# Performance work log

Hardware: AMD Instinct MI355X
Metric: run time of the kernel (lower is better)

Reference implementation:

```python
import jax, jax.numpy as jnp
from jax import lax
import numpy as np

K = 5          # conv / pool / box-filter kernel size
PAD = 2        # padding used everywhere in the module (same-size for K=5)
CO, DO = 16, 16
ROUTING = 3


def _squash(p, axis):
    # squash(p) from the source, applied along capsule-dim axis
    nsq = jnp.sum(p * p, axis=axis, keepdims=True)
    return nsq / (1.0 + nsq) * p / jnp.sqrt(nsq + 1e-9)


def setup_inputs() -> dict:
    key = jax.random.key(0)
    k1, k2 = jax.random.split(key)
    u = jax.random.normal(k1, (8, 8, 8, 48, 48), jnp.float32)          # [N,Ci,Di,H,W]
    w = jax.random.normal(k2, (8, 256, 8, 5, 5), jnp.float32) * 0.05   # [Ci,Co*Do,Di,k,k]
    return {"u": u, "w": w}


def reference(u, w):
    N, Ci, Di, H, W_ = u.shape
    # per-input-capsule convs == one grouped conv with feature_group_count=Ci
    lhs = u.reshape(N, Ci * Di, H, W_)
    rhs = w.reshape(Ci * CO * DO, Di, K, K)
    out = lax.conv_general_dilated(
        lhs, rhs, window_strides=(1, 1), padding=[(PAD, PAD), (PAD, PAD)],
        feature_group_count=Ci, dimension_numbers=("NCHW", "OIHW", "NCHW"))
    H1, W1 = out.shape[2], out.shape[3]
    u_hat = out.reshape(N, Ci, CO, DO, H1, W1)            # [N,Ci,Co,Do,H,W]

    b = jnp.zeros((N, Ci, CO, H1, W1), u.dtype)           # routing logits
    win = (1, 1, 1, K, K)
    pads = [(0, 0), (0, 0), (0, 0), (PAD, PAD), (PAD, PAD)]
    ones_strides = (1, 1, 1, 1, 1)

    v = None
    for d in range(ROUTING):
        # c_t = exp(b - maxpool2d(b).max(over Co)) : numerically-stable local softmax numerator
        bmax = lax.reduce_window(b, -jnp.inf, lax.max, win, ones_strides, pads)
        bmax = jnp.max(bmax, axis=2, keepdims=True)       # [N,Ci,1,H,W]
        c = jnp.exp(b - bmax)
        # sum_c = conv2d_same(c, ones[1,Co,k,k]) == (sum over Co) then k x k box filter (zero pad)
        sumc = lax.reduce_window(jnp.sum(c, axis=2, keepdims=True), 0.0, lax.add,
                                 win, ones_strides, pads)
        r = c / sumc                                      # [N,Ci,Co,H,W]
        uh = u_hat if d == ROUTING - 1 else lax.stop_gradient(u_hat)
        # p = sum_i r_i * u_hat_i
        p = jnp.einsum("nichw,nicdhw->ncdhw", r, uh)
        v = _squash(p, axis=2)                            # squash along Do
        if d < ROUTING - 1:
            b = b + jnp.einsum("nicdhw,ncdhw->nichw", uh, v)
    return v                                              # [N,Co,Do,H,W]
```

## Files before the change

### kernel.cpp

```cpp
#include <hip/hip_runtime.h>
#include <math.h>

#define NN  8
#define CIc 8
#define DIc 8
#define Hh  48
#define Ww  48
#define COo 16
#define DOo 16
#define HW  2304

typedef _Float16 f16x8 __attribute__((ext_vector_type(8)));
typedef _Float16 f16x4 __attribute__((ext_vector_type(4)));
typedef float f32x4 __attribute__((ext_vector_type(4)));

#define OFFB_UHAT 0
#define OFFB_B    75497472
#define OFFB_BM   84934656
#define OFFB_IS   85524480
#define OFFB_U16  86114304
#define OFFB_W16  88883200

#define PREP_U_BLOCKS 676
#define PREP_W_BLOCKS 224

__global__ __launch_bounds__(256) void prep_k(const float* __restrict__ u,
                                              const float* __restrict__ w,
                                              _Float16* __restrict__ u16,
                                              _Float16* __restrict__ w16) {
  if (blockIdx.x < PREP_U_BLOCKS) {
    int idx = blockIdx.x * 256 + threadIdx.x;
    int col = idx % 52;
    int t = idx / 52;
    int row = t % 52;
    t /= 52;
    int h = row - 2, wc = col - 2;
    f16x8 hv;
#pragma unroll
    for (int di = 0; di < 8; ++di) {
      float val = 0.f;
      if (h >= 0 && h < Hh && wc >= 0 && wc < Ww)
        val = u[((size_t)t * DIc + di) * HW + h * Ww + wc];
      hv[di] = (_Float16)val;
    }
    *(f16x8*)(u16 + (size_t)idx * 8) = hv;
  } else {
    int idx = (blockIdx.x - PREP_U_BLOCKS) * 256 + threadIdx.x;
    int tap = idx % 28;
    int t = idx / 28;
    int dd = t % DOo;
    t /= DOo;
    int co = t % COo;
    int ci = t / COo;
    f16x8 hv;
#pragma unroll
    for (int di = 0; di < 8; ++di) {
      float val = 0.f;
      if (tap < 25)
        val = w[((size_t)(ci * 256 + co * 16 + dd)) * 200 + di * 25 + tap];
      hv[di] = (_Float16)val;
    }
    *(f16x8*)(w16 + ((size_t)(ci * COo + co) * DOo + dd) * 224 + tap * 8) = hv;
  }
}

__global__ __launch_bounds__(256, 4) void conv_mfma_k(const _Float16* __restrict__ u16,
                                                      const _Float16* __restrict__ w16,
                                                      _Float16* __restrict__ uhat) {
  __shared__ _Float16 s_u[11 * 52 * 8];

  const int blk = blockIdx.x;
  const int pe = blk & 7;
  const int ch = (blk >> 3) & 1;
  const int ci = (blk >> 4) & 7;
  const int n  = blk >> 7;
  const int tid = threadIdx.x;
  const int wv = tid >> 6, lane = tid & 63;
  const int l15 = lane & 15, l4 = lane >> 4;

  const _Float16* gu = u16 + ((size_t)(n * CIc + ci) * 2704 + pe * 6 * 52) * 8;
  for (int it = tid; it < 520; it += 256)
    *(f16x8*)(s_u + it * 8) = *(const f16x8*)(gu + it * 8);
  if (tid < 52) {
    f16x8 z = {0, 0, 0, 0, 0, 0, 0, 0};
    *(f16x8*)(s_u + (520 + tid) * 8) = z;
  }

  const int co0 = ch * 8 + wv * 2;
  f16x8 a[2][7];
#pragma unroll
  for (int c = 0; c < 2; ++c) {
    const _Float16* wb = w16 + ((size_t)(ci * COo + co0 + c) * DOo + l15) * 224 + l4 * 8;
#pragma unroll
    for (int ks = 0; ks < 7; ++ks) a[c][ks] = *(const f16x8*)(wb + ks * 32);
  }
  __syncthreads();

  _Float16* ob = uhat + (size_t)((n * CIc + ci) * COo + co0) * (HW * 16);

  for (int chunk = 0; chunk < 6; ++chunk) {
    f32x4 acc[2][3];
#pragma unroll
    for (int c = 0; c < 2; ++c)
#pragma unroll
      for (int nt = 0; nt < 3; ++nt) {
        f32x4 z = {0.f, 0.f, 0.f, 0.f};
        acc[c][nt] = z;
      }
#pragma unroll
    for (int ks = 0; ks < 7; ++ks) {
      const int tap = ks * 4 + l4;
      const int dy = tap / 5;
      const int dx = tap - dy * 5;
      const int row = chunk + dy;
#pragma unroll
      for (int nt = 0; nt < 3; ++nt) {
        const int col = nt * 16 + dx + l15;
        f16x8 bfrag = *(const f16x8*)(s_u + (row * 52 + col) * 8);
        acc[0][nt] = __builtin_amdgcn_mfma_f32_16x16x32_f16(a[0][ks], bfrag, acc[0][nt], 0, 0, 0);
        acc[1][nt] = __builtin_amdgcn_mfma_f32_16x16x32_f16(a[1][ks], bfrag, acc[1][nt], 0, 0, 0);
      }
    }
#pragma unroll
    for (int c = 0; c < 2; ++c)
#pragma unroll
      for (int nt = 0; nt < 3; ++nt) {
        int p = pe * 288 + chunk * 48 + nt * 16 + l15;
        f32x4 vv = acc[c][nt];
        f16x4 hv;
        hv[0] = (_Float16)vv[0]; hv[1] = (_Float16)vv[1];
        hv[2] = (_Float16)vv[2]; hv[3] = (_Float16)vv[3];
        *(f16x4*)(ob + (size_t)c * (HW * 16) + (size_t)p * 16 + l4 * 4) = hv;
      }
  }
}

__global__ __launch_bounds__(256) void routing_stats_k(const float* __restrict__ b,
                                                       float* __restrict__ bmax,
                                                       float* __restrict__ isum) {
  __shared__ float m_lds[HW];
  __shared__ float t_lds[HW];
  const int blk = blockIdx.x;
  const int tid = threadIdx.x;
  const float* bp = b + (size_t)blk * COo * HW;

  for (int p = tid; p < HW; p += 256) {
    float m = -INFINITY;
    for (int co = 0; co < COo; ++co) m = fmaxf(m, bp[(size_t)co * HW + p]);
    m_lds[p] = m;
  }
  __syncthreads();
  for (int p = tid; p < HW; p += 256) {
    int h = p / Ww, w = p % Ww;
    float v = -INFINITY;
#pragma unroll
    for (int dx = -2; dx <= 2; ++dx) {
      int ww2 = w + dx;
      if (ww2 >= 0 && ww2 < Ww) v = fmaxf(v, m_lds[h * Ww + ww2]);
    }
    t_lds[p] = v;
  }
  __syncthreads();
  for (int p = tid; p < HW; p += 256) {
    int h = p / Ww, w = p % Ww;
    float bm = -INFINITY;
#pragma unroll
    for (int dy = -2; dy <= 2; ++dy) {
      int hh = h + dy;
      if (hh >= 0 && hh < Hh) bm = fmaxf(bm, t_lds[hh * Ww + w]);
    }
    bmax[(size_t)blk * HW + p] = bm;
    float cs = 0.f;
    for (int co = 0; co < COo; ++co)
      cs += __expf(bp[(size_t)co * HW + p] - bm);
    m_lds[p] = cs;
  }
  __syncthreads();
  for (int p = tid; p < HW; p += 256) {
    int h = p / Ww, w = p % Ww;
    float s = 0.f;
#pragma unroll
    for (int dx = -2; dx <= 2; ++dx) {
      int ww2 = w + dx;
      if (ww2 >= 0 && ww2 < Ww) s += m_lds[h * Ww + ww2];
    }
    t_lds[p] = s;
  }
  __syncthreads();
  for (int p = tid; p < HW; p += 256) {
    int h = p / Ww, w = p % Ww;
    float s = 0.f;
#pragma unroll
    for (int dy = -2; dy <= 2; ++dy) {
      int hh = h + dy;
      if (hh >= 0 && hh < Hh) s += t_lds[hh * Ww + w];
    }
    isum[(size_t)blk * HW + p] = 1.f / s;
  }
}

__global__ __launch_bounds__(256, 4) void fused_route_k(const float* __restrict__ b,
                                                        const float* __restrict__ bmax,
                                                        const float* __restrict__ isum,
                                                        const _Float16* __restrict__ uhat,
                                                        float* __restrict__ bout,
                                                        float* __restrict__ vout,
                                                        int zb, int last) {
  int idx  = blockIdx.x * 256 + threadIdx.x;
  int half = idx & 1;
  int t0   = idx >> 1;
  int p  = t0 % HW;
  int t  = t0 / HW;
  int co = t % COo;
  int n  = t / COo;

  float bl[CIc], r[CIc];
  if (zb) {
    int h = p / Ww, w = p % Ww;
    int ch = min(h + 2, Hh - 1) - max(h - 2, 0) + 1;
    int cw = min(w + 2, Ww - 1) - max(w - 2, 0) + 1;
    float r0 = 1.f / (16.f * (float)(ch * cw));
#pragma unroll
    for (int ci = 0; ci < CIc; ++ci) { bl[ci] = 0.f; r[ci] = r0; }
  } else {
#pragma unroll
    for (int ci = 0; ci < CIc; ++ci) {
      int s = n * CIc + ci;
      bl[ci] = b[(size_t)(s * COo + co) * HW + p];
      r[ci]  = __expf(bl[ci] - bmax[(size_t)s * HW + p]) * isum[(size_t)s * HW + p];
    }
  }

  float4 uh[CIc][2];
  float4 a0 = make_float4(0.f, 0.f, 0.f, 0.f);
  float4 a1 = a0;
#pragma unroll
  for (int ci = 0; ci < CIc; ++ci) {
    const f16x8* uhp = (const f16x8*)(uhat +
        ((size_t)((n * CIc + ci) * COo + co) * HW + p) * DOo + half * 8);
    f16x8 h0 = uhp[0];
    uh[ci][0] = make_float4((float)h0[0], (float)h0[1], (float)h0[2], (float)h0[3]);
    uh[ci][1] = make_float4((float)h0[4], (float)h0[5], (float)h0[6], (float)h0[7]);
    float rc = r[ci];
    a0.x = fmaf(rc, uh[ci][0].x, a0.x); a0.y = fmaf(rc, uh[ci][0].y, a0.y);
    a0.z = fmaf(rc, uh[ci][0].z, a0.z); a0.w = fmaf(rc, uh[ci][0].w, a0.w);
    a1.x = fmaf(rc, uh[ci][1].x, a1.x); a1.y = fmaf(rc, uh[ci][1].y, a1.y);
    a1.z = fmaf(rc, uh[ci][1].z, a1.z); a1.w = fmaf(rc, uh[ci][1].w, a1.w);
  }

  float nsqp = a0.x*a0.x + a0.y*a0.y + a0.z*a0.z + a0.w*a0.w
             + a1.x*a1.x + a1.y*a1.y + a1.z*a1.z + a1.w*a1.w;
  float nsq = nsqp + __shfl_xor(nsqp, 1);
  float scale = nsq / (1.f + nsq) / sqrtf(nsq + 1e-9f);
  a0.x *= scale; a0.y *= scale; a0.z *= scale; a0.w *= scale;
  a1.x *= scale; a1.y *= scale; a1.z *= scale; a1.w *= scale;

  if (last) {
    float* vp = vout + (size_t)(n * COo + co) * DOo * HW + (size_t)half * 8 * HW + p;
    vp[0*HW]=a0.x; vp[1*HW]=a0.y; vp[2*HW]=a0.z; vp[3*HW]=a0.w;
    vp[4*HW]=a1.x; vp[5*HW]=a1.y; vp[6*HW]=a1.z; vp[7*HW]=a1.w;
  } else {
#pragma unroll
    for (int ci = 0; ci < CIc; ++ci) {
      float dp = uh[ci][0].x*a0.x + uh[ci][0].y*a0.y + uh[ci][0].z*a0.z + uh[ci][0].w*a0.w
               + uh[ci][1].x*a1.x + uh[ci][1].y*a1.y + uh[ci][1].z*a1.z + uh[ci][1].w*a1.w;
      float dot = dp + __shfl_xor(dp, 1);
      if (half == 0)
        bout[(size_t)((n * CIc + ci) * COo + co) * HW + p] = bl[ci] + dot;
    }
  }
}

extern "C" void kernel_launch(void* const* d_in, const int* in_sizes, int n_in,
                              void* d_out, int out_size, void* d_ws, size_t ws_size,
                              hipStream_t stream) {
  const float* u = (const float*)d_in[0];
  const float* w = (const float*)d_in[1];
  float* out = (float*)d_out;
  char* wsb  = (char*)d_ws;

  _Float16*  uhat = (_Float16*)(wsb + OFFB_UHAT);
  float*     b    = (float*)(wsb + OFFB_B);
  float*     bm   = (float*)(wsb + OFFB_BM);
  float*     is   = (float*)(wsb + OFFB_IS);
  _Float16*  u16  = (_Float16*)(wsb + OFFB_U16);
  _Float16*  w16  = (_Float16*)(wsb + OFFB_W16);

  prep_k<<<PREP_U_BLOCKS + PREP_W_BLOCKS, 256, 0, stream>>>(u, w, u16, w16);
  conv_mfma_k<<<NN * CIc * 2 * 8, 256, 0, stream>>>(u16, w16, uhat);

  const int route_grid = (NN * COo * HW * 2) / 256;

  fused_route_k<<<route_grid, 256, 0, stream>>>(b, bm, is, uhat, b, out, 1, 0);

  routing_stats_k<<<NN * CIc, 256, 0, stream>>>(b, bm, is);
  fused_route_k<<<route_grid, 256, 0, stream>>>(b, bm, is, uhat, b, out, 0, 0);

  routing_stats_k<<<NN * CIc, 256, 0, stream>>>(b, bm, is);
  fused_route_k<<<route_grid, 256, 0, stream>>>(b, bm, is, uhat, b, out, 0, 1);
}
```

Before: 112.3 us.

## Widen conv tiles to four capsule outputs per wave and split routing threads four ways

The conv kernel now has each wave handle four output capsules instead of two. This halves the block count and reuses each shared-memory input tile across all 16 output capsules, so the duplicate input staging and LDS fragment reads are no longer repeated per half. The routing kernel now splits each 16-wide output vector across four threads instead of two. That gives more parallelism and fewer registers per thread, at the cost of an extra shuffle stage and duplicated r/b loads per thread. Occupancy bounds are adjusted for both kernels.

```diff
diff --git a/kernel.cpp b/kernel.cpp
--- a/kernel.cpp
+++ b/kernel.cpp
@@ -64,16 +64,15 @@
   }
 }
 
-__global__ __launch_bounds__(256, 4) void conv_mfma_k(const _Float16* __restrict__ u16,
+__global__ __launch_bounds__(256, 2) void conv_mfma_k(const _Float16* __restrict__ u16,
                                                       const _Float16* __restrict__ w16,
                                                       _Float16* __restrict__ uhat) {
   __shared__ _Float16 s_u[11 * 52 * 8];
 
   const int blk = blockIdx.x;
   const int pe = blk & 7;
-  const int ch = (blk >> 3) & 1;
-  const int ci = (blk >> 4) & 7;
-  const int n  = blk >> 7;
+  const int ci = (blk >> 3) & 7;
+  const int n  = blk >> 6;
   const int tid = threadIdx.x;
   const int wv = tid >> 6, lane = tid & 63;
   const int l15 = lane & 15, l4 = lane >> 4;
@@ -86,10 +85,10 @@
     *(f16x8*)(s_u + (520 + tid) * 8) = z;
   }
 
-  const int co0 = ch * 8 + wv * 2;
-  f16x8 a[2][7];
-#pragma unroll
-  for (int c = 0; c < 2; ++c) {
+  const int co0 = wv * 4;
+  f16x8 a[4][7];
+#pragma unroll
+  for (int c = 0; c < 4; ++c) {
     const _Float16* wb = w16 + ((size_t)(ci * COo + co0 + c) * DOo + l15) * 224 + l4 * 8;
 #pragma unroll
     for (int ks = 0; ks < 7; ++ks) a[c][ks] = *(const f16x8*)(wb + ks * 32);
@@ -99,9 +98,9 @@
   _Float16* ob = uhat + (size_t)((n * CIc + ci) * COo + co0) * (HW * 16);
 
   for (int chunk = 0; chunk < 6; ++chunk) {
-    f32x4 acc[2][3];
-#pragma unroll
-    for (int c = 0; c < 2; ++c)
+    f32x4 acc[4][3];
+#pragma unroll
+    for (int c = 0; c < 4; ++c)
 #pragma unroll
       for (int nt = 0; nt < 3; ++nt) {
         f32x4 z = {0.f, 0.f, 0.f, 0.f};
@@ -117,12 +116,13 @@
       for (int nt = 0; nt < 3; ++nt) {
         const int col = nt * 16 + dx + l15;
         f16x8 bfrag = *(const f16x8*)(s_u + (row * 52 + col) * 8);
-        acc[0][nt] = __builtin_amdgcn_mfma_f32_16x16x32_f16(a[0][ks], bfrag, acc[0][nt], 0, 0, 0);
-        acc[1][nt] = __builtin_amdgcn_mfma_f32_16x16x32_f16(a[1][ks], bfrag, acc[1][nt], 0, 0, 0);
+#pragma unroll
+        for (int c = 0; c < 4; ++c)
+          acc[c][nt] = __builtin_amdgcn_mfma_f32_16x16x32_f16(a[c][ks], bfrag, acc[c][nt], 0, 0, 0);
       }
     }
 #pragma unroll
-    for (int c = 0; c < 2; ++c)
+    for (int c = 0; c < 4; ++c)
 #pragma unroll
       for (int nt = 0; nt < 3; ++nt) {
         int p = pe * 288 + chunk * 48 + nt * 16 + l15;
@@ -199,16 +199,16 @@
   }
 }
 
-__global__ __launch_bounds__(256, 4) void fused_route_k(const float* __restrict__ b,
+__global__ __launch_bounds__(256, 5) void fused_route_k(const float* __restrict__ b,
                                                         const float* __restrict__ bmax,
                                                         const float* __restrict__ isum,
                                                         const _Float16* __restrict__ uhat,
                                                         float* __restrict__ bout,
                                                         float* __restrict__ vout,
                                                         int zb, int last) {
-  int idx  = blockIdx.x * 256 + threadIdx.x;
-  int half = idx & 1;
-  int t0   = idx >> 1;
+  int idx = blockIdx.x * 256 + threadIdx.x;
+  int q   = idx & 3;
+  int t0  = idx >> 2;
   int p  = t0 % HW;
   int t  = t0 / HW;
   int co = t % COo;
@@ -231,41 +231,35 @@
     }
   }
 
-  float4 uh[CIc][2];
+  float4 uh[CIc];
   float4 a0 = make_float4(0.f, 0.f, 0.f, 0.f);
-  float4 a1 = a0;
 #pragma unroll
   for (int ci = 0; ci < CIc; ++ci) {
-    const f16x8* uhp = (const f16x8*)(uhat +
-        ((size_t)((n * CIc + ci) * COo + co) * HW + p) * DOo + half * 8);
-    f16x8 h0 = uhp[0];
-    uh[ci][0] = make_float4((float)h0[0], (float)h0[1], (float)h0[2], (float)h0[3]);
-    uh[ci][1] = make_float4((float)h0[4], (float)h0[5], (float)h0[6], (float)h0[7]);
+    const f16x4* uhp = (const f16x4*)(uhat +
+        ((size_t)((n * CIc + ci) * COo + co) * HW + p) * DOo + q * 4);
+    f16x4 h0 = *uhp;
+    uh[ci] = make_float4((float)h0[0], (float)h0[1], (float)h0[2], (float)h0[3]);
     float rc = r[ci];
-    a0.x = fmaf(rc, uh[ci][0].x, a0.x); a0.y = fmaf(rc, uh[ci][0].y, a0.y);
-    a0.z = fmaf(rc, uh[ci][0].z, a0.z); a0.w = fmaf(rc, uh[ci][0].w, a0.w);
-    a1.x = fmaf(rc, uh[ci][1].x, a1.x); a1.y = fmaf(rc, uh[ci][1].y, a1.y);
-    a1.z = fmaf(rc, uh[ci][1].z, a1.z); a1.w = fmaf(rc, uh[ci][1].w, a1.w);
-  }
-
-  float nsqp = a0.x*a0.x + a0.y*a0.y + a0.z*a0.z + a0.w*a0.w
-             + a1.x*a1.x + a1.y*a1.y + a1.z*a1.z + a1.w*a1.w;
-  float nsq = nsqp + __shfl_xor(nsqp, 1);
+    a0.x = fmaf(rc, uh[ci].x, a0.x); a0.y = fmaf(rc, uh[ci].y, a0.y);
+    a0.z = fmaf(rc, uh[ci].z, a0.z); a0.w = fmaf(rc, uh[ci].w, a0.w);
+  }
+
+  float nsqp = a0.x*a0.x + a0.y*a0.y + a0.z*a0.z + a0.w*a0.w;
+  float s1  = nsqp + __shfl_xor(nsqp, 1);
+  float nsq = s1 + __shfl_xor(s1, 2);
   float scale = nsq / (1.f + nsq) / sqrtf(nsq + 1e-9f);
   a0.x *= scale; a0.y *= scale; a0.z *= scale; a0.w *= scale;
-  a1.x *= scale; a1.y *= scale; a1.z *= scale; a1.w *= scale;
 
   if (last) {
-    float* vp = vout + (size_t)(n * COo + co) * DOo * HW + (size_t)half * 8 * HW + p;
+    float* vp = vout + (size_t)(n * COo + co) * DOo * HW + (size_t)q * 4 * HW + p;
     vp[0*HW]=a0.x; vp[1*HW]=a0.y; vp[2*HW]=a0.z; vp[3*HW]=a0.w;
-    vp[4*HW]=a1.x; vp[5*HW]=a1.y; vp[6*HW]=a1.z; vp[7*HW]=a1.w;
   } else {
 #pragma unroll
     for (int ci = 0; ci < CIc; ++ci) {
-      float dp = uh[ci][0].x*a0.x + uh[ci][0].y*a0.y + uh[ci][0].z*a0.z + uh[ci][0].w*a0.w
-               + uh[ci][1].x*a1.x + uh[ci][1].y*a1.y + uh[ci][1].z*a1.z + uh[ci][1].w*a1.w;
-      float dot = dp + __shfl_xor(dp, 1);
-      if (half == 0)
+      float dp = uh[ci].x*a0.x + uh[ci].y*a0.y + uh[ci].z*a0.z + uh[ci].w*a0.w;
+      float d1 = dp + __shfl_xor(dp, 1);
+      float dot = d1 + __shfl_xor(d1, 2);
+      if (q == 0)
         bout[(size_t)((n * CIc + ci) * COo + co) * HW + p] = bl[ci] + dot;
     }
   }
@@ -287,9 +281,9 @@
   _Float16*  w16  = (_Float16*)(wsb + OFFB_W16);
 
   prep_k<<<PREP_U_BLOCKS + PREP_W_BLOCKS, 256, 0, stream>>>(u, w, u16, w16);
-  conv_mfma_k<<<NN * CIc * 2 * 8, 256, 0, stream>>>(u16, w16, uhat);
-
-  const int route_grid = (NN * COo * HW * 2) / 256;
+  conv_mfma_k<<<NN * CIc * 8, 256, 0, stream>>>(u16, w16, uhat);
+
+  const int route_grid = (NN * COo * HW * 4) / 256;
 
   fused_route_k<<<route_grid, 256, 0, stream>>>(b, bm, is, uhat, b, out, 1, 0);
 
```

Result: no change. 110.5 us (-1.6%).

## Split routing stats into row bands with halos; widen conv blocks to 4 capsules per wave

Applied to the files above, without the earlier changes.

The routing statistics kernel previously ran one block per (n, ci) slice, only 64 blocks. It now splits each slice into four 12-row bands, each recomputing a 4-row halo so the separable max and box filters stay correct, giving 256 blocks. The conv kernel now has each wave compute 4 output capsules instead of 2, halving the grid and the shared-memory input staging per output. In exchange the conv holds more registers with lower occupancy (launch bounds 2), and the stats kernel does redundant halo work.

```diff
diff --git a/kernel.cpp b/kernel.cpp
--- a/kernel.cpp
+++ b/kernel.cpp
@@ -64,16 +64,15 @@
   }
 }
 
-__global__ __launch_bounds__(256, 4) void conv_mfma_k(const _Float16* __restrict__ u16,
+__global__ __launch_bounds__(256, 2) void conv_mfma_k(const _Float16* __restrict__ u16,
                                                       const _Float16* __restrict__ w16,
                                                       _Float16* __restrict__ uhat) {
   __shared__ _Float16 s_u[11 * 52 * 8];
 
   const int blk = blockIdx.x;
   const int pe = blk & 7;
-  const int ch = (blk >> 3) & 1;
-  const int ci = (blk >> 4) & 7;
-  const int n  = blk >> 7;
+  const int ci = (blk >> 3) & 7;
+  const int n  = blk >> 6;
   const int tid = threadIdx.x;
   const int wv = tid >> 6, lane = tid & 63;
   const int l15 = lane & 15, l4 = lane >> 4;
@@ -86,10 +85,10 @@
     *(f16x8*)(s_u + (520 + tid) * 8) = z;
   }
 
-  const int co0 = ch * 8 + wv * 2;
-  f16x8 a[2][7];
-#pragma unroll
-  for (int c = 0; c < 2; ++c) {
+  const int co0 = wv * 4;
+  f16x8 a[4][7];
+#pragma unroll
+  for (int c = 0; c < 4; ++c) {
     const _Float16* wb = w16 + ((size_t)(ci * COo + co0 + c) * DOo + l15) * 224 + l4 * 8;
 #pragma unroll
     for (int ks = 0; ks < 7; ++ks) a[c][ks] = *(const f16x8*)(wb + ks * 32);
@@ -99,9 +98,9 @@
   _Float16* ob = uhat + (size_t)((n * CIc + ci) * COo + co0) * (HW * 16);
 
   for (int chunk = 0; chunk < 6; ++chunk) {
-    f32x4 acc[2][3];
-#pragma unroll
-    for (int c = 0; c < 2; ++c)
+    f32x4 acc[4][3];
+#pragma unroll
+    for (int c = 0; c < 4; ++c)
 #pragma unroll
       for (int nt = 0; nt < 3; ++nt) {
         f32x4 z = {0.f, 0.f, 0.f, 0.f};
@@ -117,12 +116,13 @@
       for (int nt = 0; nt < 3; ++nt) {
         const int col = nt * 16 + dx + l15;
         f16x8 bfrag = *(const f16x8*)(s_u + (row * 52 + col) * 8);
-        acc[0][nt] = __builtin_amdgcn_mfma_f32_16x16x32_f16(a[0][ks], bfrag, acc[0][nt], 0, 0, 0);
-        acc[1][nt] = __builtin_amdgcn_mfma_f32_16x16x32_f16(a[1][ks], bfrag, acc[1][nt], 0, 0, 0);
+#pragma unroll
+        for (int c = 0; c < 4; ++c)
+          acc[c][nt] = __builtin_amdgcn_mfma_f32_16x16x32_f16(a[c][ks], bfrag, acc[c][nt], 0, 0, 0);
       }
     }
 #pragma unroll
-    for (int c = 0; c < 2; ++c)
+    for (int c = 0; c < 4; ++c)
 #pragma unroll
       for (int nt = 0; nt < 3; ++nt) {
         int p = pe * 288 + chunk * 48 + nt * 16 + l15;
@@ -135,67 +135,74 @@
   }
 }
 
+#define BROWS 12
+#define SROWS 20
 __global__ __launch_bounds__(256) void routing_stats_k(const float* __restrict__ b,
                                                        float* __restrict__ bmax,
                                                        float* __restrict__ isum) {
-  __shared__ float m_lds[HW];
-  __shared__ float t_lds[HW];
-  const int blk = blockIdx.x;
-  const int tid = threadIdx.x;
-  const float* bp = b + (size_t)blk * COo * HW;
-
-  for (int p = tid; p < HW; p += 256) {
+  __shared__ float m_lds[SROWS * Ww];
+  __shared__ float t_lds[SROWS * Ww];
+  const int blk  = blockIdx.x;
+  const int band = blk & 3;
+  const int s    = blk >> 2;
+  const int r0   = band * BROWS;
+  const int tid  = threadIdx.x;
+  const float* bp = b + (size_t)s * COo * HW;
+
+  for (int i = tid; i < SROWS * Ww; i += 256) {
+    int sr = i / Ww, c = i % Ww;
+    int gr = r0 - 4 + sr;
     float m = -INFINITY;
-    for (int co = 0; co < COo; ++co) m = fmaxf(m, bp[(size_t)co * HW + p]);
-    m_lds[p] = m;
-  }
-  __syncthreads();
-  for (int p = tid; p < HW; p += 256) {
-    int h = p / Ww, w = p % Ww;
+    if (gr >= 0 && gr < Hh) {
+      int p = gr * Ww + c;
+      for (int co = 0; co < COo; ++co) m = fmaxf(m, bp[(size_t)co * HW + p]);
+    }
+    m_lds[i] = m;
+  }
+  __syncthreads();
+  for (int i = tid; i < SROWS * Ww; i += 256) {
+    int sr = i / Ww, c = i % Ww;
     float v = -INFINITY;
 #pragma unroll
     for (int dx = -2; dx <= 2; ++dx) {
-      int ww2 = w + dx;
-      if (ww2 >= 0 && ww2 < Ww) v = fmaxf(v, m_lds[h * Ww + ww2]);
-    }
-    t_lds[p] = v;
-  }
-  __syncthreads();
-  for (int p = tid; p < HW; p += 256) {
-    int h = p / Ww, w = p % Ww;
-    float bm = -INFINITY;
-#pragma unroll
-    for (int dy = -2; dy <= 2; ++dy) {
-      int hh = h + dy;
-      if (hh >= 0 && hh < Hh) bm = fmaxf(bm, t_lds[hh * Ww + w]);
-    }
-    bmax[(size_t)blk * HW + p] = bm;
+      int cc = c + dx;
+      if (cc >= 0 && cc < Ww) v = fmaxf(v, m_lds[sr * Ww + cc]);
+    }
+    t_lds[i] = v;
+  }
+  __syncthreads();
+  for (int i = tid; i < 16 * Ww; i += 256) {
+    int sr = i / Ww + 2, c = i % Ww;
+    float bm = fmaxf(fmaxf(fmaxf(t_lds[(sr-2)*Ww+c], t_lds[(sr-1)*Ww+c]), t_lds[sr*Ww+c]),
+                     fmaxf(t_lds[(sr+1)*Ww+c], t_lds[(sr+2)*Ww+c]));
+    int gr = r0 - 4 + sr;
     float cs = 0.f;
-    for (int co = 0; co < COo; ++co)
-      cs += __expf(bp[(size_t)co * HW + p] - bm);
-    m_lds[p] = cs;
-  }
-  __syncthreads();
-  for (int p = tid; p < HW; p += 256) {
-    int h = p / Ww, w = p % Ww;
-    float s = 0.f;
+    if (gr >= 0 && gr < Hh) {
+      int p = gr * Ww + c;
+      if (sr >= 4 && sr < 16) bmax[(size_t)s * HW + p] = bm;
+      for (int co = 0; co < COo; ++co)
+        cs += __expf(bp[(size_t)co * HW + p] - bm);
+    }
+    m_lds[sr * Ww + c] = cs;
+  }
+  __syncthreads();
+  for (int i = tid; i < 16 * Ww; i += 256) {
+    int sr = i / Ww + 2, c = i % Ww;
+    float sum = 0.f;
 #pragma unroll
     for (int dx = -2; dx <= 2; ++dx) {
-      int ww2 = w + dx;
-      if (ww2 >= 0 && ww2 < Ww) s += m_lds[h * Ww + ww2];
-    }
-    t_lds[p] = s;
-  }
-  __syncthreads();
-  for (int p = tid; p < HW; p += 256) {
-    int h = p / Ww, w = p % Ww;
-    float s = 0.f;
-#pragma unroll
-    for (int dy = -2; dy <= 2; ++dy) {
-      int hh = h + dy;
-      if (hh >= 0 && hh < Hh) s += t_lds[hh * Ww + w];
-    }
-    isum[(size_t)blk * HW + p] = 1.f / s;
+      int cc = c + dx;
+      if (cc >= 0 && cc < Ww) sum += m_lds[sr * Ww + cc];
+    }
+    t_lds[sr * Ww + c] = sum;
+  }
+  __syncthreads();
+  for (int i = tid; i < BROWS * Ww; i += 256) {
+    int sr = i / Ww + 4, c = i % Ww;
+    int gr = r0 - 4 + sr;
+    float sum = t_lds[(sr-2)*Ww+c] + t_lds[(sr-1)*Ww+c] + t_lds[sr*Ww+c]
+              + t_lds[(sr+1)*Ww+c] + t_lds[(sr+2)*Ww+c];
+    isum[(size_t)s * HW + gr * Ww + c] = 1.f / sum;
   }
 }
 
@@ -287,15 +294,16 @@
   _Float16*  w16  = (_Float16*)(wsb + OFFB_W16);
 
   prep_k<<<PREP_U_BLOCKS + PREP_W_BLOCKS, 256, 0, stream>>>(u, w, u16, w16);
-  conv_mfma_k<<<NN * CIc * 2 * 8, 256, 0, stream>>>(u16, w16, uhat);
+  conv_mfma_k<<<NN * CIc * 8, 256, 0, stream>>>(u16, w16, uhat);
 
   const int route_grid = (NN * COo * HW * 2) / 256;
+  const int stats_grid = NN * CIc * 4;
 
   fused_route_k<<<route_grid, 256, 0, stream>>>(b, bm, is, uhat, b, out, 1, 0);
 
-  routing_stats_k<<<NN * CIc, 256, 0, stream>>>(b, bm, is);
+  routing_stats_k<<<stats_grid, 256, 0, stream>>>(b, bm, is);
   fused_route_k<<<route_grid, 256, 0, stream>>>(b, bm, is, uhat, b, out, 0, 0);
 
-  routing_stats_k<<<NN * CIc, 256, 0, stream>>>(b, bm, is);
+  routing_stats_k<<<stats_grid, 256, 0, stream>>>(b, bm, is);
   fused_route_k<<<route_grid, 256, 0, stream>>>(b, bm, is, uhat, b, out, 0, 1);
 }
```

Result: faster. 92.21 us (-17.9%).
